# Kernel tuning notes

Hardware: AMD Instinct MI355X
Metric: run time of the kernel (lower is better)

## Reference

```python
import jax, jax.numpy as jnp
import numpy as np

B, S, E, H = 4, 1024, 1024, 16
D = E // H          # head_dim = 64
ROT = 32            # rotary dims (first ROT channels of each head)


def _rope(x, freqs):
    # x: [B, H, S, D]; freqs: [1, 1, S, ROT]
    r = freqs.shape[-1]
    xl, xr = x[..., :r], x[..., r:]
    half = r // 2
    rot = jnp.concatenate([-xl[..., half:], xl[..., :half]], axis=-1)  # rotate_half
    xl = xl * jnp.cos(freqs) + rot * jnp.sin(freqs)
    return jnp.concatenate([xl, xr], axis=-1)


def setup_inputs() -> dict:
    key = jax.random.key(0)
    ks = jax.random.split(key, 7)
    std = 0.02
    return {
        "hidden_states": jax.random.normal(ks[0], (B, S, E), jnp.float32),
        "rotary_pos_emb": jax.random.normal(ks[1], (1, S, ROT), jnp.float32),
        "q_w": jax.random.normal(ks[2], (E, E), jnp.float32) * std,
        "k_w": jax.random.normal(ks[3], (E, E), jnp.float32) * std,
        "v_w": jax.random.normal(ks[4], (E, E), jnp.float32) * std,
        "o_w": jax.random.normal(ks[5], (E, E), jnp.float32) * std,
        "o_b": jnp.zeros((E,), jnp.float32),
    }


def reference(hidden_states, rotary_pos_emb, q_w, k_w, v_w, o_w, o_b):
    bsz, tgt_len, embed_dim = hidden_states.shape
    scale = D ** -0.5

    def shape(t):  # [B, S, E] -> [B, H, S, D]
        return t.reshape(bsz, tgt_len, H, D).transpose(0, 2, 1, 3)

    q = shape(hidden_states @ q_w.T * scale)
    k = shape(hidden_states @ k_w.T)
    v = shape(hidden_states @ v_w.T)

    freqs = rotary_pos_emb[:, None, :, :]  # [1, 1, S, ROT]
    q = _rope(q, freqs)
    k = _rope(k, freqs)
    v = _rope(v, freqs)

    attn = jnp.einsum("bhqd,bhkd->bhqk", q, k)
    causal = jnp.tril(jnp.ones((tgt_len, tgt_len), bool))
    attn = jnp.where(causal, attn, jnp.finfo(attn.dtype).min)
    attn = jax.nn.softmax(attn, axis=-1)

    out = jnp.einsum("bhqk,bhkd->bhqd", attn, v)
    out = out.transpose(0, 2, 1, 3).reshape(bsz, tgt_len, embed_dim)
    return out @ o_w.T + o_b
```

## Files before the change

kernel.cpp:

```cpp
#include <hip/hip_runtime.h>
#include <hip/hip_bf16.h>

typedef __bf16 bf16;
typedef __attribute__((ext_vector_type(2))) __bf16 bf16x2;
typedef __attribute__((ext_vector_type(4))) __bf16 bf16x4;
typedef __attribute__((ext_vector_type(8))) __bf16 bf16x8;
typedef __attribute__((ext_vector_type(4))) float f32x4;

#define NB 4
#define NS 1024
#define NE 1024
#define NH 16
#define ND 64
#define NROT 32
#define NM (NB*NS)

__device__ __forceinline__ void gload_lds16(const bf16* g, void* l) {
  __builtin_amdgcn_global_load_lds(
      (const __attribute__((address_space(1))) unsigned int*)g,
      (__attribute__((address_space(3))) unsigned int*)l,
      16, 0, 0);
}

struct PrepArgs {
  const float* w0; const float* w1; const float* w2; const float* w3;
  bf16* b0; bf16* b1; bf16* b2; bf16* b3;
  const float* hs; bf16* hb;
  const float* rot; float* ct; float* st;
};
__global__ void k_prep(PrepArgs a) {
  const int y = blockIdx.y;
  const int i = blockIdx.x * 256 + threadIdx.x;
  if (y < 4) {
    const float* s = (y == 0) ? a.w0 : (y == 1) ? a.w1 : (y == 2) ? a.w2 : a.w3;
    bf16* d = (y == 0) ? a.b0 : (y == 1) ? a.b1 : (y == 2) ? a.b2 : a.b3;
    float4 v = reinterpret_cast<const float4*>(s)[i];
    bf16x4 o = { (bf16)v.x, (bf16)v.y, (bf16)v.z, (bf16)v.w };
    *reinterpret_cast<bf16x4*>(d + (size_t)i * 4) = o;
  } else if (y < 8) {
    size_t off = (size_t)(y - 4) * (NM * NE / 16);
    float4 v = reinterpret_cast<const float4*>(a.hs)[off + i];
    bf16x4 o = { (bf16)v.x, (bf16)v.y, (bf16)v.z, (bf16)v.w };
    *reinterpret_cast<bf16x4*>(a.hb + (off + i) * 4) = o;
  } else {
    if (i < NS * NROT) {
      float v = a.rot[i];
      a.ct[i] = cosf(v);
      a.st[i] = sinf(v);
    }
  }
}

template<bool SWAP>
__device__ __forceinline__ void gemm_core256(
    const bf16* __restrict__ A, const bf16* __restrict__ W,
    bf16* lA, bf16* lB, int m0, int n0, f32x4 (&acc)[32])
{
  const int tid = threadIdx.x;
  const int wave = tid >> 6, lane = tid & 63;
  const int wm = wave >> 2, wn = wave & 3;
  const int fr = lane & 15, kg = lane >> 4;
  const int lrow8 = lane >> 3, lslot = lane & 7;

  auto stage = [&](int kt, int c) {
#pragma unroll
    for (int i = 0; i < 4; ++i) {
      int chunk = i * 8 + wave;
      int row = (chunk << 3) + lrow8;
      int slot = lslot ^ (row & 7);
      gload_lds16(A + (size_t)(m0 + row) * NE + kt + slot * 8,
                  (char*)lA + c * 32768 + chunk * 1024);
      gload_lds16(W + (size_t)(n0 + row) * NE + kt + slot * 8,
                  (char*)lB + c * 32768 + chunk * 1024);
    }
  };

  stage(0, 0);

  for (int kt = 0; kt < NE / 64; ++kt) {
    const int c = kt & 1;
    if (kt + 1 < NE / 64) {
      stage((kt + 1) * 64, c ^ 1);
      asm volatile("s_waitcnt vmcnt(8)\n\ts_barrier" ::: "memory");
    } else {
      asm volatile("s_waitcnt vmcnt(0)\n\ts_barrier" ::: "memory");
    }

    const char* cA = (const char*)lA + c * 32768;
    const char* cB = (const char*)lB + c * 32768;
#pragma unroll
    for (int kk = 0; kk < 2; ++kk) {
      bf16x8 af[8], bfr[4];
#pragma unroll
      for (int i = 0; i < 8; ++i) {
        int ra = wm * 128 + i * 16 + fr;
        af[i] = *reinterpret_cast<const bf16x8*>(cA + ra * 128 + (((kg + 4 * kk) ^ (ra & 7)) << 4));
      }
#pragma unroll
      for (int j = 0; j < 4; ++j) {
        int rb = wn * 64 + j * 16 + fr;
        bfr[j] = *reinterpret_cast<const bf16x8*>(cB + rb * 128 + (((kg + 4 * kk) ^ (rb & 7)) << 4));
      }
#pragma unroll
      for (int i = 0; i < 8; ++i)
#pragma unroll
        for (int j = 0; j < 4; ++j) {
          if constexpr (SWAP)
            acc[j * 8 + i] = __builtin_amdgcn_mfma_f32_16x16x32_bf16(bfr[j], af[i], acc[j * 8 + i], 0, 0, 0);
          else
            acc[i * 4 + j] = __builtin_amdgcn_mfma_f32_16x16x32_bf16(af[i], bfr[j], acc[i * 4 + j], 0, 0, 0);
        }
    }
    asm volatile("s_waitcnt lgkmcnt(0)\n\ts_barrier" ::: "memory");
  }
}

__global__ __launch_bounds__(512, 2) void k_proj(
    const bf16* __restrict__ A, const bf16* __restrict__ Wq, const bf16* __restrict__ Wk,
    const bf16* __restrict__ Wv, bf16* __restrict__ Oq, bf16* __restrict__ Ok,
    bf16* __restrict__ vt, const float* __restrict__ ct, const float* __restrict__ st)
{
  __shared__ bf16 lA[2 * 256 * 64];
  __shared__ bf16 lB[2 * 256 * 64];
  const int z = blockIdx.z;
  const int m0 = blockIdx.x * 256, n0 = blockIdx.y * 256;
  const int tid = threadIdx.x;
  const int wave = tid >> 6, lane = tid & 63;
  const int wm = wave >> 2, wn = wave & 3;
  const int fr = lane & 15, kg = lane >> 4;

  f32x4 acc[32] = {};

  if (z == 2) {
    gemm_core256<true>(A, Wv, lA, lB, m0, n0, acc);

    const int b = m0 >> 10;
    const int h = (n0 + wn * 64) >> 6;
    bf16* vtb = vt + ((size_t)(b * 16 + h)) * ND * NS;
#pragma unroll
    for (int i = 0; i < 8; ++i) {
      int sl = (m0 & (NS - 1)) + wm * 128 + i * 16 + fr;
#pragma unroll
      for (int r = 0; r < 4; ++r) {
        int dbase = kg * 4 + r;
        float x0 = acc[0 * 8 + i][r];
        float x1 = acc[1 * 8 + i][r];
        float c0 = ct[sl * NROT + dbase],      sn0 = st[sl * NROT + dbase];
        float c1 = ct[sl * NROT + 16 + dbase], sn1 = st[sl * NROT + 16 + dbase];
        float y0 = x0 * c0 - x1 * sn0;
        float y1 = x1 * c1 + x0 * sn1;
        vtb[(size_t)(dbase)      * NS + sl] = (bf16)y0;
        vtb[(size_t)(16 + dbase) * NS + sl] = (bf16)y1;
        vtb[(size_t)(32 + dbase) * NS + sl] = (bf16)acc[2 * 8 + i][r];
        vtb[(size_t)(48 + dbase) * NS + sl] = (bf16)acc[3 * 8 + i][r];
      }
    }
  } else {
    const bf16* W = (z == 0) ? Wq : Wk;
    bf16* Og = (z == 0) ? Oq : Ok;
    const float scale = (z == 0) ? 0.125f * 1.44269504f : 1.0f;

    gemm_core256<false>(A, W, lA, lB, m0, n0, acc);

#pragma unroll
    for (int i = 0; i < 8; ++i) {
      int rowbase = m0 + wm * 128 + i * 16 + kg * 4;
#pragma unroll
      for (int r = 0; r < 4; ++r) {
        int gm = rowbase + r;
        int s = gm & (NS - 1);
        float x0 = acc[i * 4 + 0][r] * scale;
        float x1 = acc[i * 4 + 1][r] * scale;
        float c0 = ct[s * NROT + fr],      sn0 = st[s * NROT + fr];
        float c1 = ct[s * NROT + 16 + fr], sn1 = st[s * NROT + 16 + fr];
        float y0 = x0 * c0 - x1 * sn0;
        float y1 = x1 * c1 + x0 * sn1;
        size_t rb = (size_t)gm * NE + n0 + wn * 64;
        Og[rb + 0 * 16 + fr] = (bf16)y0;
        Og[rb + 1 * 16 + fr] = (bf16)y1;
        Og[rb + 2 * 16 + fr] = (bf16)(acc[i * 4 + 2][r] * scale);
        Og[rb + 3 * 16 + fr] = (bf16)(acc[i * 4 + 3][r] * scale);
      }
    }
  }
}

template<int BM, int BN>
__device__ __forceinline__ void gemm_core(
    const bf16* __restrict__ A, const bf16* __restrict__ W,
    bf16* lA, bf16* lB, int m0, int n0, f32x4 (&acc)[BM/32][BN/32])
{
  const int tid = threadIdx.x;
  const int wave = tid >> 6, lane = tid & 63;
  const int wm = wave >> 1, wn = wave & 1;
  const int fr = lane & 15, kg = lane >> 4;

  const int sline = lane >> 3;
  const int lsl   = (lane & 7) ^ sline;
  const int srow  = 2 * sline + (lsl >> 2);
  const int skcol = (lsl & 3) * 8;
  constexpr int ACH = BM / 64;
  constexpr int BCH = BN / 64;
  constexpr int NSTAGE = ACH + BCH;

  auto stage = [&](int kt, int c) {
#pragma unroll
    for (int i = 0; i < ACH; ++i) {
      int chunk = i * 4 + wave;
      gload_lds16(A + (size_t)(m0 + chunk * 16 + srow) * NE + kt + skcol,
                  (char*)lA + c * (BM * 64) + chunk * 1024);
    }
#pragma unroll
    for (int i = 0; i < BCH; ++i) {
      int chunk = i * 4 + wave;
      gload_lds16(W + (size_t)(n0 + chunk * 16 + srow) * NE + kt + skcol,
                  (char*)lB + c * (BN * 64) + chunk * 1024);
    }
  };

  auto foff = [&](int ra) {
    return (ra >> 1) * 128 + (((((ra & 1) << 2) + kg) ^ ((ra >> 1) & 7)) << 4);
  };

  stage(0, 0);

  for (int kt = 0; kt < NE / 32; ++kt) {
    const int c = kt & 1;
    if (kt + 1 < NE / 32) {
      stage((kt + 1) * 32, c ^ 1);
      asm volatile("s_waitcnt vmcnt(%0)\n\ts_barrier" :: "n"(NSTAGE) : "memory");
    } else {
      asm volatile("s_waitcnt vmcnt(0)\n\ts_barrier" ::: "memory");
    }

    const char* cA = (const char*)lA + c * (BM * 64);
    const char* cB = (const char*)lB + c * (BN * 64);
    bf16x8 af[BM / 32], bfr[BN / 32];
#pragma unroll
    for (int i = 0; i < BM / 32; ++i)
      af[i] = *reinterpret_cast<const bf16x8*>(cA + foff(wm * (BM / 2) + i * 16 + fr));
#pragma unroll
    for (int j = 0; j < BN / 32; ++j)
      bfr[j] = *reinterpret_cast<const bf16x8*>(cB + foff(wn * (BN / 2) + j * 16 + fr));
#pragma unroll
    for (int i = 0; i < BM / 32; ++i)
#pragma unroll
      for (int j = 0; j < BN / 32; ++j)
        acc[i][j] = __builtin_amdgcn_mfma_f32_16x16x32_bf16(af[i], bfr[j], acc[i][j], 0, 0, 0);
    asm volatile("s_waitcnt lgkmcnt(0)\n\ts_barrier" ::: "memory");
  }
}

__global__ __launch_bounds__(256) void k_gemm_o(
    const bf16* __restrict__ A, const bf16* __restrict__ W, float* __restrict__ Og,
    const float* __restrict__ bias)
{
  __shared__ bf16 lA[2 * 64 * 32];
  __shared__ bf16 lB[2 * 128 * 32];
  const int m0 = blockIdx.x * 64, n0 = blockIdx.y * 128;
  f32x4 acc[2][4] = {};
  gemm_core<64, 128>(A, W, lA, lB, m0, n0, acc);

  const int tid = threadIdx.x;
  const int wave = tid >> 6, lane = tid & 63;
  const int wm = wave >> 1, wn = wave & 1;
  const int fr = lane & 15, kg = lane >> 4;
#pragma unroll
  for (int i = 0; i < 2; ++i)
#pragma unroll
    for (int j = 0; j < 4; ++j) {
      int gc = n0 + wn * 64 + j * 16 + fr;
      float bv = bias[gc];
#pragma unroll
      for (int r = 0; r < 4; ++r) {
        int gm = m0 + wm * 32 + i * 16 + kg * 4 + r;
        Og[(size_t)gm * NE + gc] = acc[i][j][r] + bv;
      }
    }
}

__global__ __launch_bounds__(256) void k_attn(
    const bf16* __restrict__ Q, const bf16* __restrict__ K,
    const bf16* __restrict__ VT, bf16* __restrict__ O)
{
  __shared__ bf16 lK[2][64 * 64];
  __shared__ bf16 lVT[64 * 64];
  __shared__ bf16 lP[4][16 * 68];
  const int tid = threadIdx.x;
  const int wave = tid >> 6, lane = tid & 63;
  const int fr = lane & 15, kg = lane >> 4;

  const int qt = 15 - (blockIdx.y >> 3);
  const int bh = blockIdx.x | ((blockIdx.y & 7) << 3);
  const int b = bh >> 4, h = bh & 15;
  const int nt = qt + 1;
  const bf16* Qb  = Q + (size_t)b * NS * NE + h * 64;
  const bf16* Kb  = K + (size_t)b * NS * NE + h * 64;
  const bf16* VTb = VT + (size_t)bh * ND * NS;
  bf16* Ob = O + (size_t)b * NS * NE + h * 64;

  const int qrow0 = qt * 64 + wave * 16;

  bf16x8 qf[2];
#pragma unroll
  for (int kk = 0; kk < 2; ++kk)
    qf[kk] = *reinterpret_cast<const bf16x8*>(
        Qb + (size_t)(qrow0 + fr) * NE + kk * 32 + kg * 8);

  const int srow = lane >> 3;
  const int sslot = (lane & 7) ^ srow;
  const int r0 = wave * 8 + srow;
  const int r1 = (wave + 4) * 8 + srow;
  const bf16* kA0 = Kb + (size_t)r0 * NE + sslot * 8;
  const bf16* kA1 = Kb + (size_t)r1 * NE + sslot * 8;
  const bf16* vA0 = VTb + (size_t)r0 * NS + sslot * 8;
  const bf16* vA1 = VTb + (size_t)r1 * NS + sslot * 8;
  char* ldsKa[2] = { (char*)lK[0] + wave * 1024, (char*)lK[1] + wave * 1024 };
  char* ldsKb[2] = { (char*)lK[0] + (wave + 4) * 1024, (char*)lK[1] + (wave + 4) * 1024 };
  char* ldsVa  = (char*)lVT + wave * 1024;
  char* ldsVb  = (char*)lVT + (wave + 4) * 1024;

  float m_ = -3.0e38f, l_ = 0.f;
  f32x4 oacc[4] = {};

  gload_lds16(kA0, ldsKa[0]);
  gload_lds16(kA1, ldsKb[0]);
  __syncthreads();

  for (int t = 0; t < nt; ++t) {
    const int c = t & 1;
    gload_lds16(vA0 + t * 64, ldsVa);
    gload_lds16(vA1 + t * 64, ldsVb);
    if (t + 1 < nt) {
      gload_lds16(kA0 + (size_t)(t + 1) * 64 * NE, ldsKa[c ^ 1]);
      gload_lds16(kA1 + (size_t)(t + 1) * 64 * NE, ldsKb[c ^ 1]);
    }

    const bf16* lKc = lK[c];
    f32x4 sacc[4] = {};
    __builtin_amdgcn_s_setprio(1);
#pragma unroll
    for (int kk = 0; kk < 2; ++kk)
#pragma unroll
      for (int j = 0; j < 4; ++j) {
        int rc = j * 16 + fr;
        bf16x8 kf = *reinterpret_cast<const bf16x8*>(
            lKc + rc * 64 + (((kg + 4 * kk) ^ (rc & 7)) << 3));
        sacc[j] = __builtin_amdgcn_mfma_f32_16x16x32_bf16(kf, qf[kk], sacc[j], 0, 0, 0);
      }
    __builtin_amdgcn_s_setprio(0);

    if (t == qt) {
      const int ql = wave * 16 + fr;
#pragma unroll
      for (int j = 0; j < 4; ++j)
#pragma unroll
        for (int r = 0; r < 4; ++r)
          if (16 * j + 4 * kg + r > ql) sacc[j][r] = -3.0e38f;
    }

    float m4 = fmaxf(fmaxf(fmaxf(sacc[0][0], sacc[0][1]), fmaxf(sacc[0][2], sacc[0][3])),
                     fmaxf(fmaxf(sacc[1][0], sacc[1][1]), fmaxf(sacc[1][2], sacc[1][3])));
    m4 = fmaxf(m4, fmaxf(fmaxf(fmaxf(sacc[2][0], sacc[2][1]), fmaxf(sacc[2][2], sacc[2][3])),
                         fmaxf(fmaxf(sacc[3][0], sacc[3][1]), fmaxf(sacc[3][2], sacc[3][3]))));
    m4 = fmaxf(m4, __shfl_xor(m4, 16));
    m4 = fmaxf(m4, __shfl_xor(m4, 32));

    if (!__all(m4 - m_ <= 8.0f)) {
      float nm = fmaxf(m_, m4);
      float corr = exp2f(m_ - nm);
      m_ = nm;
      l_ *= corr;
#pragma unroll
      for (int r = 0; r < 4; ++r) {
        float cr = __shfl(corr, kg * 4 + r);
#pragma unroll
        for (int df = 0; df < 4; ++df) oacc[df][r] *= cr;
      }
    }

    float ps = 0.f;
#pragma unroll
    for (int j = 0; j < 4; ++j) {
      float p0 = exp2f(sacc[j][0] - m_);
      float p1 = exp2f(sacc[j][1] - m_);
      float p2 = exp2f(sacc[j][2] - m_);
      float p3 = exp2f(sacc[j][3] - m_);
      ps += (p0 + p1) + (p2 + p3);
      bf16x4 pp = { (bf16)p0, (bf16)p1, (bf16)p2, (bf16)p3 };
      *reinterpret_cast<bf16x4*>(&lP[wave][fr * 68 + j * 16 + kg * 4]) = pp;
    }
    ps += __shfl_xor(ps, 16);
    ps += __shfl_xor(ps, 32);
    l_ += ps;

    __syncthreads();

    __builtin_amdgcn_s_setprio(1);
#pragma unroll
    for (int ks = 0; ks < 2; ++ks) {
      bf16x8 pf = *reinterpret_cast<const bf16x8*>(&lP[wave][fr * 68 + ks * 32 + kg * 8]);
#pragma unroll
      for (int df = 0; df < 4; ++df) {
        int d = df * 16 + fr;
        bf16x8 vf = *reinterpret_cast<const bf16x8*>(
            (const bf16*)lVT + d * 64 + (((kg + 4 * ks) ^ (d & 7)) << 3));
        oacc[df] = __builtin_amdgcn_mfma_f32_16x16x32_bf16(pf, vf, oacc[df], 0, 0, 0);
      }
    }
    __builtin_amdgcn_s_setprio(0);

    __syncthreads();
  }

  float linv[4];
#pragma unroll
  for (int r = 0; r < 4; ++r) linv[r] = 1.0f / __shfl(l_, kg * 4 + r);
#pragma unroll
  for (int df = 0; df < 4; ++df)
#pragma unroll
    for (int r = 0; r < 4; ++r)
      Ob[(size_t)(qrow0 + kg * 4 + r) * NE + df * 16 + fr] = (bf16)(oacc[df][r] * linv[r]);
}

extern "C" void kernel_launch(void* const* d_in, const int* in_sizes, int n_in,
                              void* d_out, int out_size, void* d_ws, size_t ws_size,
                              hipStream_t stream) {
  const float* hs  = (const float*)d_in[0];
  const float* rot = (const float*)d_in[1];
  const float* qw  = (const float*)d_in[2];
  const float* kw  = (const float*)d_in[3];
  const float* vw  = (const float*)d_in[4];
  const float* ow  = (const float*)d_in[5];
  const float* obb = (const float*)d_in[6];
  float* out = (float*)d_out;

  char* ws = (char*)d_ws;
  size_t off = 0;
  bf16* hb  = (bf16*)(ws + off); off += (size_t)NM * NE * 2;
  bf16* wqb = (bf16*)(ws + off); off += (size_t)NE * NE * 2;
  bf16* wkb = (bf16*)(ws + off); off += (size_t)NE * NE * 2;
  bf16* wvb = (bf16*)(ws + off); off += (size_t)NE * NE * 2;
  bf16* wob = (bf16*)(ws + off); off += (size_t)NE * NE * 2;
  bf16* qb  = (bf16*)(ws + off); off += (size_t)NM * NE * 2;
  bf16* kb  = (bf16*)(ws + off); off += (size_t)NM * NE * 2;
  bf16* vt  = (bf16*)(ws + off); off += (size_t)NM * NE * 2;
  float* ct = (float*)(ws + off); off += (size_t)NS * NROT * 4;
  float* st = (float*)(ws + off); off += (size_t)NS * NROT * 4;
  bf16* aob = hb;

  PrepArgs pa = { qw, kw, vw, ow, wqb, wkb, wvb, wob, hs, hb, rot, ct, st };
  k_prep<<<dim3(NE * NE / 4 / 256, 9), dim3(256), 0, stream>>>(pa);

  k_proj<<<dim3(NM / 256, NE / 256, 3), dim3(512), 0, stream>>>(
      hb, wqb, wkb, wvb, qb, kb, vt, ct, st);

  k_attn<<<dim3(8, 128), dim3(256), 0, stream>>>(qb, kb, vt, aob);

  k_gemm_o<<<dim3(NM / 64, NE / 128), dim3(256), 0, stream>>>(aob, wob, out, obb);

  (void)in_sizes; (void)n_in; (void)out_size; (void)ws_size;
}
```

Before: 105.3 us.

## Interleave next-tile global loads with MFMA sub-steps in projection GEMM

The GEMM main loop of the QKV projection is restructured so the next K-tile's global-to-LDS copies are issued in four quarters, each interleaved with a slice of MFMA work, instead of all at once before compute. B fragments are loaded once per tile and A fragments per quarter, with sched_barrier and setprio marking the MFMA regions to raise their priority. The launch bound drops the minimum-occupancy hint of 2 blocks per CU, giving the compiler more registers but possibly lowering occupancy. The goal is better overlap of memory traffic with matrix math and less register pressure from holding all A fragments at once.

Measured after the change: 101.7 us. 3.5% less time.

```diff
diff --git a/kernel.cpp b/kernel.cpp
--- a/kernel.cpp
+++ b/kernel.cpp
@@ -62,60 +62,89 @@
   const int fr = lane & 15, kg = lane >> 4;
   const int lrow8 = lane >> 3, lslot = lane & 7;
 
-  auto stage = [&](int kt, int c) {
-#pragma unroll
-    for (int i = 0; i < 4; ++i) {
-      int chunk = i * 8 + wave;
+  auto stageH = [&](int kt, int c, int h) {
+    const bf16* src = (h < 2) ? A : W;
+    bf16* dst = (h < 2) ? lA : lB;
+    const int base0 = (h < 2) ? m0 : n0;
+    const int hh = h & 1;
+#pragma unroll
+    for (int i = 0; i < 2; ++i) {
+      int chunk = hh * 16 + i * 8 + wave;
       int row = (chunk << 3) + lrow8;
       int slot = lslot ^ (row & 7);
-      gload_lds16(A + (size_t)(m0 + row) * NE + kt + slot * 8,
-                  (char*)lA + c * 32768 + chunk * 1024);
-      gload_lds16(W + (size_t)(n0 + row) * NE + kt + slot * 8,
-                  (char*)lB + c * 32768 + chunk * 1024);
+      gload_lds16(src + (size_t)(base0 + row) * NE + kt + slot * 8,
+                  (char*)dst + c * 32768 + chunk * 1024);
     }
   };
 
-  stage(0, 0);
-
-  for (int kt = 0; kt < NE / 64; ++kt) {
-    const int c = kt & 1;
-    if (kt + 1 < NE / 64) {
-      stage((kt + 1) * 64, c ^ 1);
-      asm volatile("s_waitcnt vmcnt(8)\n\ts_barrier" ::: "memory");
-    } else {
-      asm volatile("s_waitcnt vmcnt(0)\n\ts_barrier" ::: "memory");
-    }
-
+#pragma unroll
+  for (int h = 0; h < 4; ++h) stageH(0, 0, h);
+  asm volatile("s_waitcnt vmcnt(0)\n\ts_barrier" ::: "memory");
+
+  constexpr int NT = NE / 64;
+  bf16x8 bfrag[4][2];
+
+  for (int t = 0; t < NT; ++t) {
+    const int c = t & 1;
     const char* cA = (const char*)lA + c * 32768;
     const char* cB = (const char*)lB + c * 32768;
-#pragma unroll
-    for (int kk = 0; kk < 2; ++kk) {
-      bf16x8 af[8], bfr[4];
-#pragma unroll
-      for (int i = 0; i < 8; ++i) {
-        int ra = wm * 128 + i * 16 + fr;
-        af[i] = *reinterpret_cast<const bf16x8*>(cA + ra * 128 + (((kg + 4 * kk) ^ (ra & 7)) << 4));
-      }
-#pragma unroll
-      for (int j = 0; j < 4; ++j) {
-        int rb = wn * 64 + j * 16 + fr;
-        bfr[j] = *reinterpret_cast<const bf16x8*>(cB + rb * 128 + (((kg + 4 * kk) ^ (rb & 7)) << 4));
-      }
-#pragma unroll
-      for (int i = 0; i < 8; ++i)
+
+#pragma unroll
+    for (int q = 0; q < 4; ++q) {
+      if (t + 1 < NT) stageH((t + 1) * 64, c ^ 1, q);
+
+      if (q == 0) {
+        if (t > 0) {
+          if (t + 1 < NT)
+            asm volatile("s_waitcnt vmcnt(2)\n\ts_barrier" ::: "memory");
+          else
+            asm volatile("s_waitcnt vmcnt(0)\n\ts_barrier" ::: "memory");
+        }
 #pragma unroll
         for (int j = 0; j < 4; ++j) {
-          if constexpr (SWAP)
-            acc[j * 8 + i] = __builtin_amdgcn_mfma_f32_16x16x32_bf16(bfr[j], af[i], acc[j * 8 + i], 0, 0, 0);
-          else
-            acc[i * 4 + j] = __builtin_amdgcn_mfma_f32_16x16x32_bf16(af[i], bfr[j], acc[i * 4 + j], 0, 0, 0);
+          int rb = wn * 64 + j * 16 + fr;
+#pragma unroll
+          for (int kk = 0; kk < 2; ++kk)
+            bfrag[j][kk] = *reinterpret_cast<const bf16x8*>(
+                cB + rb * 128 + (((kg + 4 * kk) ^ (rb & 7)) << 4));
         }
-    }
+      }
+
+      bf16x8 af[2][2];
+#pragma unroll
+      for (int u = 0; u < 2; ++u) {
+        int ra = wm * 128 + (2 * q + u) * 16 + fr;
+#pragma unroll
+        for (int kk = 0; kk < 2; ++kk)
+          af[u][kk] = *reinterpret_cast<const bf16x8*>(
+              cA + ra * 128 + (((kg + 4 * kk) ^ (ra & 7)) << 4));
+      }
+
+      __builtin_amdgcn_sched_barrier(0);
+      __builtin_amdgcn_s_setprio(1);
+#pragma unroll
+      for (int kk = 0; kk < 2; ++kk)
+#pragma unroll
+        for (int u = 0; u < 2; ++u)
+#pragma unroll
+          for (int j = 0; j < 4; ++j) {
+            const int i = 2 * q + u;
+            if constexpr (SWAP)
+              acc[j * 8 + i] = __builtin_amdgcn_mfma_f32_16x16x32_bf16(
+                  bfrag[j][kk], af[u][kk], acc[j * 8 + i], 0, 0, 0);
+            else
+              acc[i * 4 + j] = __builtin_amdgcn_mfma_f32_16x16x32_bf16(
+                  af[u][kk], bfrag[j][kk], acc[i * 4 + j], 0, 0, 0);
+          }
+      __builtin_amdgcn_s_setprio(0);
+      __builtin_amdgcn_sched_barrier(0);
+    }
+
     asm volatile("s_waitcnt lgkmcnt(0)\n\ts_barrier" ::: "memory");
   }
 }
 
-__global__ __launch_bounds__(512, 2) void k_proj(
+__global__ __launch_bounds__(512) void k_proj(
     const bf16* __restrict__ A, const bf16* __restrict__ Wq, const bf16* __restrict__ Wk,
     const bf16* __restrict__ Wv, bf16* __restrict__ Oq, bf16* __restrict__ Ok,
     bf16* __restrict__ vt, const float* __restrict__ ct, const float* __restrict__ st)
```
